# Kernel tuning notes

Measured on AMD Instinct MI355X. Metric: run time of the kernel, lower is better.

Reference implementation:

```python
import jax, jax.numpy as jnp
import numpy as np

N = 50000        # nodes
E = 800000       # edges (edge-nodes of the line graph)
LGE = 1600000    # line-graph edges
F_NODE = 256     # node feature dim
T = 64           # timestamp/edge feature dim
HID = 128        # hidden size
OUT = 64         # out size
SLOPE = 0.2      # leaky relu negative slope used in EdgeGCN / attention


def _glorot(key, shape):
    lim = jnp.sqrt(6.0 / (shape[0] + shape[1]))
    return jax.random.uniform(key, shape, jnp.float32, -lim, lim)


def setup_inputs() -> dict:
    key = jax.random.key(0)
    ks = jax.random.split(key, 24)
    inp = {
        "x": jax.random.normal(ks[0], (N, F_NODE), jnp.float32),
        "et": jax.random.normal(ks[1], (E, T), jnp.float32),
        "H": jax.random.randint(ks[2], (2, E), 0, N),
        "raw_edge_index": jax.random.randint(ks[3], (2, E), 0, N),
        "lg_edge_index": jax.random.randint(ks[4], (2, LGE), 0, E),
        # TSAEncoder: two SAGE-style layers on the line graph (T->HID->HID)
        "W_tsa1_s": _glorot(ks[5], (T, HID)),
        "W_tsa1_n": _glorot(ks[6], (T, HID)),
        "W_tsa2_s": _glorot(ks[7], (HID, HID)),
        "W_tsa2_n": _glorot(ks[8], (HID, HID)),
        # EdgeToNodeConv + EdgeGCN output linear
        "W_etn": _glorot(ks[9], (HID, HID)),
        "W_eg_lin": _glorot(ks[10], (HID, HID)),
        # edge_aggr SAGE (num_layers-1 = 1 layer)
        "W_ea_s": _glorot(ks[11], (HID, HID)),
        "W_ea_n": _glorot(ks[12], (HID, HID)),
        # attr_node_model SAGE (2 layers)
        "W_an1_s": _glorot(ks[13], (F_NODE, HID)),
        "W_an1_n": _glorot(ks[14], (F_NODE, HID)),
        "W_an2_s": _glorot(ks[15], (HID, HID)),
        "W_an2_n": _glorot(ks[16], (HID, HID)),
        # MixAttention
        "Wq": _glorot(ks[17], (HID, HID)),
        "Wk": _glorot(ks[18], (HID, HID)),
        "Wv": _glorot(ks[19], (HID, HID)),
        # final classifier
        "W_out": _glorot(ks[20], (HID, OUT)),
    }
    return inp


def _sage(h, src, dst, Ws, Wn, n):
    # mean-aggregator SAGE conv: self transform + mean of in-neighbors
    deg = jnp.clip(jax.ops.segment_sum(jnp.ones(src.shape[0], h.dtype), dst, num_segments=n), 1.0)
    nbr = jax.ops.segment_sum(h[src], dst, num_segments=n) / deg[:, None]
    return h @ Ws + nbr @ Wn


def reference(x, et, H, raw_edge_index, lg_edge_index,
              W_tsa1_s, W_tsa1_n, W_tsa2_s, W_tsa2_n,
              W_etn, W_eg_lin, W_ea_s, W_ea_n,
              W_an1_s, W_an1_n, W_an2_s, W_an2_n,
              Wq, Wk, Wv, W_out):
    src_lg, dst_lg = lg_edge_index[0], lg_edge_index[1]
    src, dst = raw_edge_index[0], raw_edge_index[1]

    # ---- EdgeGCN: TSAEncoder over line graph (edges as nodes) ----
    h = jax.nn.relu(_sage(et, src_lg, dst_lg, W_tsa1_s, W_tsa1_n, E))
    h = _sage(h, src_lg, dst_lg, W_tsa2_s, W_tsa2_n, E)          # [E, HID]

    # ---- EdgeToNodeConv: scatter edge reprs to both incident nodes (mean) ----
    ones_e = jnp.ones(E, h.dtype)
    agg = (jax.ops.segment_sum(h, H[0], num_segments=N)
           + jax.ops.segment_sum(h, H[1], num_segments=N))        # [N, HID]
    deg = jnp.clip(jax.ops.segment_sum(ones_e, H[0], num_segments=N)
                   + jax.ops.segment_sum(ones_e, H[1], num_segments=N), 1.0)
    node_e = (agg / deg[:, None]) @ W_etn
    edge_repr = jax.nn.leaky_relu(node_e, negative_slope=SLOPE) @ W_eg_lin  # [N, HID]

    # ---- edge_aggr: 1-layer SAGE over raw graph ----
    aggr_edge = _sage(edge_repr, src, dst, W_ea_s, W_ea_n, N)     # [N, HID]

    # ---- attr_node_model: 2-layer SAGE ----
    hn = jax.nn.relu(_sage(x, src, dst, W_an1_s, W_an1_n, N))
    hn = _sage(hn, src, dst, W_an2_s, W_an2_n, N)                 # [N, HID]

    # ---- MixAttention: edge-indexed cross attention (node queries, edge-repr keys/values) ----
    q = hn @ Wq
    k = aggr_edge @ Wk
    v = aggr_edge @ Wv
    score = jax.nn.leaky_relu(
        jnp.sum(q[dst] * k[src], axis=-1) / jnp.sqrt(jnp.asarray(HID, q.dtype)),
        negative_slope=SLOPE)                                     # [E]
    m = jax.ops.segment_max(score, dst, num_segments=N)
    m = jnp.where(jnp.isfinite(m), m, 0.0)
    ex = jnp.exp(score - m[dst])
    den = jnp.clip(jax.ops.segment_sum(ex, dst, num_segments=N), 1e-9)
    alpha = ex / den[dst]
    out = hn + jax.ops.segment_sum(alpha[:, None] * v[src], dst, num_segments=N)

    return jax.nn.log_softmax(out @ W_out, axis=1)                # [N, OUT]
```

## Files before the change

### kernel.cpp

```cpp
#include <hip/hip_runtime.h>
#include <cstddef>

static constexpr int Nn   = 50000;
static constexpr int Ee   = 800000;
static constexpr int LGEe = 1600000;

typedef __attribute__((ext_vector_type(8))) short bf16x8;
typedef __attribute__((ext_vector_type(4))) float f32x4;

__device__ __forceinline__ float bf2f(unsigned int u16) {
  return __uint_as_float(u16 << 16);
}
__device__ __forceinline__ unsigned int f2bf(float f) {
  unsigned int u = __float_as_uint(f);
  u += 0x7fffu + ((u >> 16) & 1u);
  return u >> 16;
}

__global__ __launch_bounds__(256)
void k_count_direct(const int* __restrict__ idx, int* __restrict__ cnt, int n) {
  int i = blockIdx.x * 256 + threadIdx.x;
  if (i < n) atomicAdd(&cnt[idx[i]], 1);
}
__global__ __launch_bounds__(256)
void k_count_comp(const int* __restrict__ Hrow, const int* __restrict__ dlg,
                  int* __restrict__ cnt, int n) {
  int i = blockIdx.x * 256 + threadIdx.x;
  if (i < n) atomicAdd(&cnt[Hrow[dlg[i]]], 1);
}
__global__ __launch_bounds__(256)
void k_scan1(const int* __restrict__ in, int* __restrict__ out,
             int* __restrict__ bsum, int n) {
  __shared__ int sd[256];
  int tid = threadIdx.x;
  int base = blockIdx.x * 1024 + tid * 4;
  int4 v = {0, 0, 0, 0};
  if (base < n) v = *(const int4*)(in + base);
  int s = v.x + v.y + v.z + v.w;
  sd[tid] = s; __syncthreads();
  for (int off = 1; off < 256; off <<= 1) {
    int t_ = (tid >= off) ? sd[tid - off] : 0; __syncthreads();
    sd[tid] += t_; __syncthreads();
  }
  int excl = sd[tid] - s;
  if (base < n) {
    int4 o; o.x = excl; o.y = o.x + v.x; o.z = o.y + v.y; o.w = o.z + v.z;
    *(int4*)(out + base) = o;
  }
  if (tid == 255) bsum[blockIdx.x] = sd[255];
}
__global__ __launch_bounds__(1024)
void k_scan2(int* __restrict__ b, int nb) {
  __shared__ int sd[1024];
  int tid = threadIdx.x;
  int v = (tid < nb) ? b[tid] : 0;
  sd[tid] = v; __syncthreads();
  for (int off = 1; off < 1024; off <<= 1) {
    int t_ = (tid >= off) ? sd[tid - off] : 0; __syncthreads();
    sd[tid] += t_; __syncthreads();
  }
  if (tid < nb) b[tid] = sd[tid] - v;
}
__global__ __launch_bounds__(256)
void k_scan3(int* __restrict__ out, const int* __restrict__ bsum, int n, int total) {
  int i = blockIdx.x * 256 + threadIdx.x;
  if (i < n) out[i] += bsum[i >> 10];
  if (i == 0) out[n] = total;
}
__global__ __launch_bounds__(256)
void k_fillA(const int* __restrict__ dlg, const int* __restrict__ slg,
             const int* __restrict__ ptr, int* __restrict__ cur,
             int* __restrict__ ent, int n) {
  int m = blockIdx.x * 256 + threadIdx.x;
  if (m >= n) return;
  int d = dlg[m];
  int pos = ptr[d] + atomicAdd(&cur[d], 1);
  ent[pos] = slg[m];
}
__global__ __launch_bounds__(256)
void k_fillB(const int* __restrict__ Hrow, const int* __restrict__ dlg,
             const int* __restrict__ slg, const int* __restrict__ ptrA,
             const int* __restrict__ ptrB, int* __restrict__ cur,
             int* __restrict__ entS, float* __restrict__ entW, int n) {
  int m = blockIdx.x * 256 + threadIdx.x;
  if (m >= n) return;
  int d = dlg[m];
  int seg = Hrow[d];
  int pos = ptrB[seg] + atomicAdd(&cur[seg], 1);
  entS[pos] = slg[m];
  int la = ptrA[d + 1] - ptrA[d];
  entW[pos] = 1.0f / (float)max(la, 1);
}
__global__ __launch_bounds__(256)
void k_fillC(const int* __restrict__ Hrow, const int* __restrict__ ptr,
             int* __restrict__ cur, int* __restrict__ ent, int n) {
  int e = blockIdx.x * 256 + threadIdx.x;
  if (e >= n) return;
  int seg = Hrow[e];
  int pos = ptr[seg] + atomicAdd(&cur[seg], 1);
  ent[pos] = e;
}
__global__ __launch_bounds__(256)
void k_fillD(const int* __restrict__ dstA, const int* __restrict__ srcA,
             const int* __restrict__ ptr, int* __restrict__ cur,
             int* __restrict__ ent, int n) {
  int e = blockIdx.x * 256 + threadIdx.x;
  if (e >= n) return;
  int seg = dstA[e];
  int pos = ptr[seg] + atomicAdd(&cur[seg], 1);
  ent[pos] = srcA[e];
}
__global__ __launch_bounds__(256)
void k_rdeg(const int* __restrict__ ptr, float* __restrict__ r, int n) {
  int i = blockIdx.x * 256 + threadIdx.x;
  if (i < n) r[i] = 1.0f / fmaxf((float)(ptr[i + 1] - ptr[i]), 1.0f);
}

__global__ __launch_bounds__(256)
void k_gemm128(int M, const float* __restrict__ A, int K,
               const float* __restrict__ W, const float* __restrict__ dgA,
               int reluA, int act, float* __restrict__ C, int beta)
{
  __shared__ float sA[32][132];
  __shared__ float sW[32][132];
  const int t = threadIdx.x, tr = t >> 4, tc = t & 15;
  const int row0 = blockIdx.x * 128;
  float acc[8][8];
  #pragma unroll
  for (int i = 0; i < 8; ++i)
    #pragma unroll
    for (int j = 0; j < 8; ++j) acc[i][j] = 0.f;

  #pragma unroll 1
  for (int k0 = 0; k0 < K; k0 += 32) {
    __syncthreads();
    #pragma unroll
    for (int j = 0; j < 4; ++j) {
      int idx = t * 4 + j * 1024;
      int r = idx >> 5, kk = idx & 31;
      int gr = row0 + r; if (gr > M - 1) gr = M - 1;
      float4 va = *(const float4*)(A + (size_t)gr * K + k0 + kk);
      if (reluA) {
        va.x = fmaxf(va.x, 0.f); va.y = fmaxf(va.y, 0.f);
        va.z = fmaxf(va.z, 0.f); va.w = fmaxf(va.w, 0.f);
      }
      if (dgA) {
        float sc = dgA[gr];
        va.x *= sc; va.y *= sc; va.z *= sc; va.w *= sc;
      }
      sA[kk + 0][r] = va.x; sA[kk + 1][r] = va.y;
      sA[kk + 2][r] = va.z; sA[kk + 3][r] = va.w;
    }
    #pragma unroll
    for (int j = 0; j < 4; ++j) {
      int idx = t * 4 + j * 1024;
      int kk = idx >> 7, c = idx & 127;
      *(float4*)&sW[kk][c] = *(const float4*)(W + (size_t)(k0 + kk) * 128 + c);
    }
    __syncthreads();
    #pragma unroll
    for (int kk = 0; kk < 32; ++kk) {
      float a[8], w[8];
      *(float4*)&a[0] = *(const float4*)&sA[kk][tr * 4];
      *(float4*)&a[4] = *(const float4*)&sA[kk][64 + tr * 4];
      *(float4*)&w[0] = *(const float4*)&sW[kk][tc * 4];
      *(float4*)&w[4] = *(const float4*)&sW[kk][64 + tc * 4];
      #pragma unroll
      for (int i = 0; i < 8; ++i)
        #pragma unroll
        for (int j = 0; j < 8; ++j)
          acc[i][j] = fmaf(a[i], w[j], acc[i][j]);
    }
  }
  #pragma unroll 1
  for (int i = 0; i < 8; ++i) {
    int gr = row0 + (i & 4) * 16 + tr * 4 + (i & 3);
    if (gr >= M) continue;
    float o[8];
    #pragma unroll
    for (int j = 0; j < 8; ++j) {
      float vv = acc[i][j];
      if (act == 1)      vv = fmaxf(vv, 0.f);
      else if (act == 2) vv = vv > 0.f ? vv : vv * 0.2f;
      o[j] = vv;
    }
    float* p = C + (size_t)gr * 128;
    if (beta) {
      float4 c0 = *(const float4*)(p + tc * 4), c1 = *(const float4*)(p + 64 + tc * 4);
      o[0] += c0.x; o[1] += c0.y; o[2] += c0.z; o[3] += c0.w;
      o[4] += c1.x; o[5] += c1.y; o[6] += c1.z; o[7] += c1.w;
    }
    *(float4*)(p + tc * 4)      = *(const float4*)&o[0];
    *(float4*)(p + 64 + tc * 4) = *(const float4*)&o[4];
  }
}

__global__ __launch_bounds__(256)
void k_tsa1(const float* __restrict__ et,
            const int* __restrict__ rp, const int* __restrict__ ent,
            const float* __restrict__ Ws, const float* __restrict__ Wn,
            unsigned short* __restrict__ BUF)
{
  __shared__ __align__(16) unsigned char smem[34816];
  unsigned short* sAh = (unsigned short*)smem;
  unsigned short* sAl = (unsigned short*)(smem + 16384);
  int*   sEnt  = (int*)(smem + 32768);
  float* stage = (float*)smem;

  const int t = threadIdx.x, wv = t >> 6, lane = t & 63;
  const int tr = t >> 4, tc = t & 15;
  const int nrow = lane & 15, kg = lane >> 4;
  const int seg0 = blockIdx.x * 64;
  const int segbase = seg0 + wv * 16;

  int rpv = (lane <= 16) ? rp[segbase + lane] : 0;
  int nxtv = __shfl(rpv, (lane + 1) & 63);
  float invv = 1.f / fmaxf((float)(nxtv - rpv), 1.f);

  const int base = rp[seg0];
  const int cnt  = rp[seg0 + 64] - base;
  const int lim  = cnt < 512 ? cnt : 512;
  for (int i = t; i < lim; i += 256) sEnt[i] = ent[base + i];

  {
    float dv[16];
    #pragma unroll
    for (int i = 0; i < 16; ++i)
      dv[i] = et[(size_t)(segbase + i) * 64 + lane];
    #pragma unroll
    for (int i = 0; i < 16; ++i) {
      int ss = wv * 16 + i;
      unsigned int hi = f2bf(dv[i]);
      float lo = dv[i] - bf2f(hi);
      int idx = ss * 128 + (lane ^ ((ss & 7) << 3));
      sAh[idx] = (unsigned short)hi;
      sAl[idx] = (unsigned short)f2bf(lo);
    }
  }

  bf16x8 Bh[2][4], Bl[2][4];
  #pragma unroll
  for (int np = 0; np < 2; ++np) {
    int n = (wv * 2 + np) * 16 + nrow;
    #pragma unroll
    for (int kc = 0; kc < 4; ++kc) {
      const float* Wp = (kc < 2) ? Ws : Wn;
      int kr0 = (kc & 1) * 32 + kg * 8;
      #pragma unroll
      for (int j = 0; j < 8; ++j) {
        float w = Wp[(size_t)(kr0 + j) * 128 + n];
        unsigned int hi = f2bf(w);
        float lo = w - bf2f(hi);
        Bh[np][kc][j] = (short)(unsigned short)hi;
        Bl[np][kc][j] = (short)(unsigned short)f2bf(lo);
      }
    }
  }
  __syncthreads();

  {
    int q0 = __shfl(rpv, 0);
    int q1 = __shfl(rpv, 16);
    int c = 0;
    int b_next = __shfl(rpv, 1);
    float idg = __shfl(invv, 0);
    float a = 0.f;
    #pragma unroll 1
    for (int j = q0; j < q1; j += 8) {
      float x[8];
      #pragma unroll
      for (int u = 0; u < 8; ++u) {
        int jj = j + u; jj = jj < q1 ? jj : q1 - 1;
        int ix = jj - base;
        int s = (ix < 512) ? sEnt[ix] : ent[jj];
        x[u] = et[(size_t)s * 64 + lane];
      }
      #pragma unroll
      for (int u = 0; u < 8; ++u) {
        int jj = j + u;
        if (jj >= q1) break;
        while (jj >= b_next) {
          float v = a * idg;
          int ss = wv * 16 + c;
          unsigned int hi = f2bf(v);
          float lo = v - bf2f(hi);
          int idx = ss * 128 + ((64 + lane) ^ ((ss & 7) << 3));
          sAh[idx] = (unsigned short)hi;
          sAl[idx] = (unsigned short)f2bf(lo);
          a = 0.f;
          ++c;
          b_next = __shfl(rpv, c + 1);
          idg = __shfl(invv, c);
        }
        a += x[u];
      }
    }
    #pragma unroll 1
    for (;;) {
      float v = a * idg;
      int ss = wv * 16 + c;
      unsigned int hi = f2bf(v);
      float lo = v - bf2f(hi);
      int idx = ss * 128 + ((64 + lane) ^ ((ss & 7) << 3));
      sAh[idx] = (unsigned short)hi;
      sAl[idx] = (unsigned short)f2bf(lo);
      a = 0.f;
      if (++c >= 16) break;
      idg = __shfl(invv, c);
    }
  }
  __syncthreads();

  f32x4 acc[4][2];
  #pragma unroll
  for (int m = 0; m < 4; ++m)
    #pragma unroll
    for (int np = 0; np < 2; ++np)
      acc[m][np] = (f32x4){0.f, 0.f, 0.f, 0.f};

  #pragma unroll
  for (int kc = 0; kc < 4; ++kc) {
    #pragma unroll
    for (int m = 0; m < 4; ++m) {
      int ss = m * 16 + nrow;
      int kbase = kc * 32 + kg * 8;
      int idx = ss * 128 + (kbase ^ ((ss & 7) << 3));
      bf16x8 ah = *(const bf16x8*)(sAh + idx);
      bf16x8 al = *(const bf16x8*)(sAl + idx);
      #pragma unroll
      for (int np = 0; np < 2; ++np) {
        acc[m][np] = __builtin_amdgcn_mfma_f32_16x16x32_bf16(ah, Bh[np][kc], acc[m][np], 0, 0, 0);
        acc[m][np] = __builtin_amdgcn_mfma_f32_16x16x32_bf16(al, Bh[np][kc], acc[m][np], 0, 0, 0);
        acc[m][np] = __builtin_amdgcn_mfma_f32_16x16x32_bf16(ah, Bl[np][kc], acc[m][np], 0, 0, 0);
      }
    }
  }

  __syncthreads();
  #pragma unroll
  for (int m = 0; m < 4; ++m)
    #pragma unroll
    for (int np = 0; np < 2; ++np)
      #pragma unroll
      for (int r = 0; r < 4; ++r)
        stage[(m * 16 + kg * 4 + r) * 132 + (wv * 2 + np) * 16 + nrow] = acc[m][np][r];
  __syncthreads();
  #pragma unroll
  for (int i = 0; i < 4; ++i) {
    int s = tr * 4 + i;
    const float* sp = stage + s * 132 + tc * 8;
    float4 v0 = *(const float4*)sp;
    float4 v1 = *(const float4*)(sp + 4);
    unsigned int pk[4];
    pk[0] = f2bf(v0.x) | (f2bf(v0.y) << 16);
    pk[1] = f2bf(v0.z) | (f2bf(v0.w) << 16);
    pk[2] = f2bf(v1.x) | (f2bf(v1.y) << 16);
    pk[3] = f2bf(v1.z) | (f2bf(v1.w) << 16);
    uint4 st = {pk[0], pk[1], pk[2], pk[3]};
    *(uint4*)(BUF + (size_t)(seg0 + s) * 128 + tc * 8) = st;
  }
}

__global__ __launch_bounds__(256)
void k_poolb(const int* __restrict__ rp, const int* __restrict__ ent,
             const float* __restrict__ entw,
             const unsigned short* __restrict__ SRC,
             float* __restrict__ O, int nseg, int total)
{
  const int wv = threadIdx.x >> 6, lane = threadIdx.x & 63;
  const int chunk = blockIdx.x * 4 + wv;
  const int c0 = chunk * 256;
  if (c0 >= total) return;
  int c1 = c0 + 256; if (c1 > total) c1 = total;

  int lo = 0, hi = nseg;
  while (lo + 1 < hi) {
    int mid = (lo + hi) >> 1;
    if (rp[mid] <= c0) lo = mid; else hi = mid;
  }
  int seg = lo;
  int sstart = rp[seg];
  int send = rp[seg + 1];
  float a0 = 0.f, a1 = 0.f;

  #pragma unroll 1
  for (int j = c0; j < c1; j += 8) {
    int ids[8]; float w[8];
    #pragma unroll
    for (int u = 0; u < 8; ++u) {
      int jj = j + u; jj = jj < c1 ? jj : c1 - 1;
      ids[u] = ent[jj];
      w[u] = entw ? entw[jj] : 1.f;
    }
    unsigned int uv[8];
    #pragma unroll
    for (int u = 0; u < 8; ++u)
      uv[u] = *(const unsigned int*)(SRC + (size_t)ids[u] * 128 + 2 * lane);
    #pragma unroll
    for (int u = 0; u < 8; ++u) {
      int jj = j + u;
      if (jj >= c1) break;
      while (jj >= send) {
        float* p = O + (size_t)seg * 128;
        if (sstart >= c0 && send <= c1) {
          p[2 * lane]     += a0;
          p[2 * lane + 1] += a1;
        } else {
          atomicAdd(p + 2 * lane, a0);
          atomicAdd(p + 2 * lane + 1, a1);
        }
        a0 = a1 = 0.f;
        ++seg; sstart = send; send = rp[seg + 1];
      }
      a0 = fmaf(w[u], fmaxf(bf2f(uv[u] & 0xffffu), 0.f), a0);
      a1 = fmaf(w[u], fmaxf(bf2f(uv[u] >> 16),     0.f), a1);
    }
  }
  {
    float* p = O + (size_t)seg * 128;
    if (sstart >= c0 && send <= c1) {
      p[2 * lane]     += a0;
      p[2 * lane + 1] += a1;
    } else {
      atomicAdd(p + 2 * lane, a0);
      atomicAdd(p + 2 * lane + 1, a1);
    }
  }
}

__global__ __launch_bounds__(256)
void k_poolf(const int* __restrict__ rp, const int* __restrict__ ent,
             const float* __restrict__ SRC, float* __restrict__ O,
             int nseg, int total)
{
  const int wv = threadIdx.x >> 6, lane = threadIdx.x & 63;
  const int chunk = blockIdx.x * 4 + wv;
  const int c0 = chunk * 256;
  if (c0 >= total) return;
  int c1 = c0 + 256; if (c1 > total) c1 = total;

  int lo = 0, hi = nseg;
  while (lo + 1 < hi) {
    int mid = (lo + hi) >> 1;
    if (rp[mid] <= c0) lo = mid; else hi = mid;
  }
  int seg = lo;
  int sstart = rp[seg];
  int send = rp[seg + 1];
  float a0 = 0.f, a1 = 0.f;

  #pragma unroll 1
  for (int j = c0; j < c1; j += 8) {
    int ids[8];
    #pragma unroll
    for (int u = 0; u < 8; ++u) {
      int jj = j + u; jj = jj < c1 ? jj : c1 - 1;
      ids[u] = ent[jj];
    }
    float2 v[8];
    #pragma unroll
    for (int u = 0; u < 8; ++u)
      v[u] = ((const float2*)(SRC + (size_t)ids[u] * 128))[lane];
    #pragma unroll
    for (int u = 0; u < 8; ++u) {
      int jj = j + u;
      if (jj >= c1) break;
      while (jj >= send) {
        float sc = 1.f / fmaxf((float)(send - sstart), 1.f);
        float* p = O + (size_t)seg * 128;
        if (sstart >= c0 && send <= c1) {
          p[2 * lane]     += a0 * sc;
          p[2 * lane + 1] += a1 * sc;
        } else {
          atomicAdd(p + 2 * lane, a0 * sc);
          atomicAdd(p + 2 * lane + 1, a1 * sc);
        }
        a0 = a1 = 0.f;
        ++seg; sstart = send; send = rp[seg + 1];
      }
      a0 += v[u].x; a1 += v[u].y;
    }
  }
  {
    float sc = 1.f / fmaxf((float)(send - sstart), 1.f);
    float* p = O + (size_t)seg * 128;
    if (sstart >= c0 && send <= c1) {
      p[2 * lane]     += a0 * sc;
      p[2 * lane + 1] += a1 * sc;
    } else {
      atomicAdd(p + 2 * lane, a0 * sc);
      atomicAdd(p + 2 * lane + 1, a1 * sc);
    }
  }
}

__global__ __launch_bounds__(256)
void k_attn(const int* __restrict__ rp, const int* __restrict__ ent,
            const float* __restrict__ q, const float* __restrict__ kb,
            const float* __restrict__ vb, float* __restrict__ o, int nseg)
{
  int wv = threadIdx.x >> 6, lane = threadIdx.x & 63;
  int seg = blockIdx.x * 4 + wv;
  if (seg >= nseg) return;
  int p0 = rp[seg], p1 = rp[seg + 1];
  if (p0 >= p1) return;
  float2 q2 = ((const float2*)(q + (size_t)seg * 128))[lane];
  float m = -1e30f, l = 0.f, o0 = 0.f, o1 = 0.f;
  #pragma unroll 1
  for (int j = p0; j < p1; j += 4) {
    int s[4];
    #pragma unroll
    for (int i = 0; i < 4; ++i) {
      int jj = j + i; jj = jj < p1 ? jj : p1 - 1;
      s[i] = ent[jj];
    }
    float2 k2[4], v2[4];
    #pragma unroll
    for (int i = 0; i < 4; ++i)
      k2[i] = ((const float2*)(kb + (size_t)s[i] * 128))[lane];
    #pragma unroll
    for (int i = 0; i < 4; ++i)
      v2[i] = ((const float2*)(vb + (size_t)s[i] * 128))[lane];
    float d[4];
    #pragma unroll
    for (int i = 0; i < 4; ++i) d[i] = fmaf(q2.x, k2[i].x, q2.y * k2[i].y);
    #pragma unroll
    for (int off = 1; off < 64; off <<= 1) {
      #pragma unroll
      for (int i = 0; i < 4; ++i) d[i] += __shfl_xor(d[i], off);
    }
    float sc[4];
    #pragma unroll
    for (int i = 0; i < 4; ++i) {
      float v = d[i] * 0.088388347648318447f;
      v = v > 0.f ? v : 0.2f * v;
      sc[i] = (j + i < p1) ? v : -1e30f;
    }
    float mb = fmaxf(fmaxf(sc[0], sc[1]), fmaxf(sc[2], sc[3]));
    float mn = fmaxf(m, mb);
    float scale = expf(m - mn);
    float e[4];
    #pragma unroll
    for (int i = 0; i < 4; ++i)
      e[i] = (j + i < p1) ? expf(sc[i] - mn) : 0.f;
    l  = l  * scale + ((e[0] + e[1]) + (e[2] + e[3]));
    o0 = o0 * scale + ((e[0] * v2[0].x + e[1] * v2[1].x) + (e[2] * v2[2].x + e[3] * v2[3].x));
    o1 = o1 * scale + ((e[0] * v2[0].y + e[1] * v2[1].y) + (e[2] * v2[2].y + e[3] * v2[3].y));
    m = mn;
  }
  float inv = 1.f / fmaxf(l, 1e-9f);
  float2* orow = (float2*)(o + (size_t)seg * 128);
  float2 cur = orow[lane];
  cur.x += o0 * inv; cur.y += o1 * inv;
  orow[lane] = cur;
}

__global__ __launch_bounds__(256)
void k_out(const float* __restrict__ attn, const float* __restrict__ Wout,
           float* __restrict__ out, int n) {
  __shared__ float sW[128 * 64];
  for (int i = threadIdx.x; i < 128 * 64; i += 256) sW[i] = Wout[i];
  __syncthreads();
  int wave = threadIdx.x >> 6, lane = threadIdx.x & 63;
  int row = blockIdx.x * 4 + wave;
  if (row >= n) return;
  const float* a = attn + (size_t)row * 128;
  float z = 0.f;
  #pragma unroll 8
  for (int k = 0; k < 128; ++k) z = fmaf(a[k], sW[k * 64 + lane], z);
  float mx = z;
  #pragma unroll
  for (int off = 32; off; off >>= 1) mx = fmaxf(mx, __shfl_xor(mx, off));
  float ee = expf(z - mx);
  float ss = ee;
  #pragma unroll
  for (int off = 32; off; off >>= 1) ss += __shfl_xor(ss, off);
  out[(size_t)row * 64 + lane] = z - mx - logf(ss);
}

extern "C" void kernel_launch(void* const* d_in, const int* in_sizes, int n_in,
                              void* d_out, int out_size, void* d_ws, size_t ws_size,
                              hipStream_t stream) {
  (void)in_sizes; (void)n_in; (void)out_size;
  const float* x        = (const float*)d_in[0];
  const float* et       = (const float*)d_in[1];
  const int*   H0       = (const int*)d_in[2];
  const int*   H1       = H0 + Ee;
  const int*   src      = (const int*)d_in[3];
  const int*   dst      = src + Ee;
  const int*   src_lg   = (const int*)d_in[4];
  const int*   dst_lg   = src_lg + LGEe;
  const float* W_tsa1_s = (const float*)d_in[5];
  const float* W_tsa1_n = (const float*)d_in[6];
  const float* W_tsa2_s = (const float*)d_in[7];
  const float* W_tsa2_n = (const float*)d_in[8];
  const float* W_etn    = (const float*)d_in[9];
  const float* W_eg_lin = (const float*)d_in[10];
  const float* W_ea_s   = (const float*)d_in[11];
  const float* W_ea_n   = (const float*)d_in[12];
  const float* W_an1_s  = (const float*)d_in[13];
  const float* W_an1_n  = (const float*)d_in[14];
  const float* W_an2_s  = (const float*)d_in[15];
  const float* W_an2_n  = (const float*)d_in[16];
  const float* Wq       = (const float*)d_in[17];
  const float* Wk       = (const float*)d_in[18];
  const float* Wv       = (const float*)d_in[19];
  const float* W_out    = (const float*)d_in[20];
  float* out = (float*)d_out;

  char* wp = (char*)d_ws;
  size_t avail = ws_size;
  auto alloc = [&](size_t bytes) -> void* {
    void* r = (void*)wp;
    size_t pad = (bytes + 255) & ~(size_t)255;
    wp += pad; avail = (avail >= pad) ? avail - pad : 0;
    return r;
  };
  const size_t NH = (size_t)Nn * 128;
  unsigned short* BUF = (unsigned short*)alloc((size_t)Ee * 128 * 2);
  float* agg   = (float*)alloc(NH * 4);
  int* ptrA  = (int*)alloc(((size_t)Ee + 1) * 4);
  int* cntA  = (int*)alloc((size_t)Ee * 4);
  int* entA  = (int*)alloc((size_t)LGEe * 4);
  int* ptrB  = (int*)alloc(((size_t)Nn + 1) * 4);
  int* cntB  = (int*)alloc((size_t)Nn * 4);
  int* entBs = (int*)alloc((size_t)2 * LGEe * 4);
  float* entBw = (float*)alloc((size_t)2 * LGEe * 4);
  int* ptrC  = (int*)alloc(((size_t)Nn + 1) * 4);
  int* cntC  = (int*)alloc((size_t)Nn * 4);
  int* entC  = (int*)alloc((size_t)2 * Ee * 4);
  int* ptrD  = (int*)alloc(((size_t)Nn + 1) * 4);
  int* cntD  = (int*)alloc((size_t)Nn * 4);
  int* entD  = (int*)alloc((size_t)Ee * 4);
  float* rdegN = (float*)alloc((size_t)Nn * 4);
  int* bsum  = (int*)alloc(2048 * 4);
  if (avail == 0 && wp > (char*)d_ws + ws_size) return;

  float* er  = (float*)BUF + 0 * NH;
  float* ae  = (float*)BUF + 1 * NH;
  float* hn  = (float*)BUF + 2 * NH;
  float* hn2 = (float*)BUF + 3 * NH;
  float* qb  = (float*)BUF + 4 * NH;
  float* kb  = (float*)BUF + 5 * NH;
  float* vb  = (float*)BUF + 6 * NH;
  float* tmp = (float*)BUF + 7 * NH;
  float* T = (float*)entBs;

  auto cdiv = [](long a, long b) { return (int)((a + b - 1) / b); };
  auto scan = [&](int* cnt, int* ptr, int n, int total) {
    int nb = cdiv(n, 1024);
    k_scan1<<<nb, 256, 0, stream>>>(cnt, ptr, bsum, n);
    k_scan2<<<1, 1024, 0, stream>>>(bsum, nb);
    k_scan3<<<cdiv(n, 256), 256, 0, stream>>>(ptr, bsum, n, total);
  };

  const int gLG = cdiv(LGEe, 256), gEe = cdiv(Ee, 256);

  hipMemsetAsync(cntA, 0, (size_t)Ee * 4, stream);
  k_count_direct<<<gLG, 256, 0, stream>>>(dst_lg, cntA, LGEe);
  scan(cntA, ptrA, Ee, LGEe);
  hipMemsetAsync(cntA, 0, (size_t)Ee * 4, stream);
  k_fillA<<<gLG, 256, 0, stream>>>(dst_lg, src_lg, ptrA, cntA, entA, LGEe);

  hipMemsetAsync(cntB, 0, (size_t)Nn * 4, stream);
  k_count_comp<<<gLG, 256, 0, stream>>>(H0, dst_lg, cntB, LGEe);
  k_count_comp<<<gLG, 256, 0, stream>>>(H1, dst_lg, cntB, LGEe);
  scan(cntB, ptrB, Nn, 2 * LGEe);
  hipMemsetAsync(cntB, 0, (size_t)Nn * 4, stream);
  k_fillB<<<gLG, 256, 0, stream>>>(H0, dst_lg, src_lg, ptrA, ptrB, cntB, entBs, entBw, LGEe);
  k_fillB<<<gLG, 256, 0, stream>>>(H1, dst_lg, src_lg, ptrA, ptrB, cntB, entBs, entBw, LGEe);

  hipMemsetAsync(cntC, 0, (size_t)Nn * 4, stream);
  k_count_direct<<<gEe, 256, 0, stream>>>(H0, cntC, Ee);
  k_count_direct<<<gEe, 256, 0, stream>>>(H1, cntC, Ee);
  scan(cntC, ptrC, Nn, 2 * Ee);
  hipMemsetAsync(cntC, 0, (size_t)Nn * 4, stream);
  k_fillC<<<gEe, 256, 0, stream>>>(H0, ptrC, cntC, entC, Ee);
  k_fillC<<<gEe, 256, 0, stream>>>(H1, ptrC, cntC, entC, Ee);

  hipMemsetAsync(cntD, 0, (size_t)Nn * 4, stream);
  k_count_direct<<<gEe, 256, 0, stream>>>(dst, cntD, Ee);
  scan(cntD, ptrD, Nn, Ee);
  hipMemsetAsync(cntD, 0, (size_t)Nn * 4, stream);
  k_fillD<<<gEe, 256, 0, stream>>>(dst, src, ptrD, cntD, entD, Ee);
  k_rdeg<<<cdiv(Nn, 256), 256, 0, stream>>>(ptrC, rdegN, Nn);

  const int gN128 = cdiv(Nn, 128);
  const int gW    = cdiv(Nn, 4);
  const int gP2   = cdiv(cdiv(2 * LGEe, 256), 4);
  const int gP1   = cdiv(cdiv(2 * Ee, 256), 4);
  const int gPf   = cdiv(cdiv(Ee, 256), 4);

  k_tsa1<<<Ee / 64, 256, 0, stream>>>(et, ptrA, entA, W_tsa1_s, W_tsa1_n, BUF);

  hipMemsetAsync(agg, 0, NH * 4, stream);
  k_poolb<<<gP2, 256, 0, stream>>>(ptrB, entBs, entBw, BUF, agg, Nn, 2 * LGEe);
  k_gemm128<<<gN128, 256, 0, stream>>>(Nn, agg, 128, W_tsa2_n, nullptr, 0, 0, T, 0);
  hipMemsetAsync(agg, 0, NH * 4, stream);
  k_poolb<<<gP1, 256, 0, stream>>>(ptrC, entC, nullptr, BUF, agg, Nn, 2 * Ee);
  k_gemm128<<<gN128, 256, 0, stream>>>(Nn, agg, 128, W_tsa2_s, nullptr, 0, 0, T, 1);
  k_gemm128<<<gN128, 256, 0, stream>>>(Nn, T, 128, W_etn, rdegN, 0, 2, tmp, 0);
  k_gemm128<<<gN128, 256, 0, stream>>>(Nn, tmp, 128, W_eg_lin, nullptr, 0, 0, er, 0);

  k_gemm128<<<gN128, 256, 0, stream>>>(Nn, er, 128, W_ea_s, nullptr, 0, 0, ae, 0);
  k_gemm128<<<gN128, 256, 0, stream>>>(Nn, er, 128, W_ea_n, nullptr, 0, 0, tmp, 0);
  k_poolf<<<gPf, 256, 0, stream>>>(ptrD, entD, tmp, ae, Nn, Ee);

  k_gemm128<<<gN128, 256, 0, stream>>>(Nn, x, 256, W_an1_s, nullptr, 0, 0, hn, 0);
  k_gemm128<<<gN128, 256, 0, stream>>>(Nn, x, 256, W_an1_n, nullptr, 0, 0, tmp, 0);
  k_poolf<<<gPf, 256, 0, stream>>>(ptrD, entD, tmp, hn, Nn, Ee);
  k_gemm128<<<gN128, 256, 0, stream>>>(Nn, hn, 128, W_an2_s, nullptr, 1, 0, hn2, 0);
  k_gemm128<<<gN128, 256, 0, stream>>>(Nn, hn, 128, W_an2_n, nullptr, 1, 0, tmp, 0);
  k_poolf<<<gPf, 256, 0, stream>>>(ptrD, entD, tmp, hn2, Nn, Ee);

  k_gemm128<<<gN128, 256, 0, stream>>>(Nn, hn2, 128, Wq, nullptr, 0, 0, qb, 0);
  k_gemm128<<<gN128, 256, 0, stream>>>(Nn, ae, 128, Wk, nullptr, 0, 0, kb, 0);
  k_gemm128<<<gN128, 256, 0, stream>>>(Nn, ae, 128, Wv, nullptr, 0, 0, vb, 0);
  k_attn<<<gW, 256, 0, stream>>>(ptrD, entD, qb, kb, vb, hn2, Nn);

  k_out<<<gW, 256, 0, stream>>>(hn2, W_out, out, Nn);
}
```

Measured before the change: 2.812 ms.

## Replace FP32 SIMT GEMMs with split-bf16 MFMA kernel and fuse paired GEMMs

Swaps the scalar FP32 128x128-tiled GEMM for a kernel that runs 16x16x32 bf16 MFMA instructions. Each FP32 operand is split into a bf16 high part and a bf16 residual, and three MFMAs per step recover near-FP32 accuracy. A DUAL template variant multiplies the same A tile by two weight matrices, so the paired self/neighbor and K/V GEMMs read A once and need fewer launches. Weights are reloaded from global memory and split again in every block, which adds conversion overhead, and the result carries a small precision risk compared with plain FP32.

```diff
diff --git a/kernel.cpp b/kernel.cpp
--- a/kernel.cpp
+++ b/kernel.cpp
@@ -116,30 +116,79 @@
   if (i < n) r[i] = 1.0f / fmaxf((float)(ptr[i + 1] - ptr[i]), 1.0f);
 }
 
-__global__ __launch_bounds__(256)
-void k_gemm128(int M, const float* __restrict__ A, int K,
-               const float* __restrict__ W, const float* __restrict__ dgA,
-               int reluA, int act, float* __restrict__ C, int beta)
+#define MG_SWEEP(WP, ACC)                                                       \
+  {                                                                             \
+    bf16x8 Bh[2][4], Bl[2][4];                                                  \
+    _Pragma("unroll")                                                           \
+    for (int np = 0; np < 2; ++np) {                                            \
+      int n = (wv * 2 + np) * 16 + nrow;                                        \
+      _Pragma("unroll")                                                         \
+      for (int kc = 0; kc < 4; ++kc) {                                          \
+        int kr0 = kh * 128 + kc * 32 + kg * 8;                                  \
+        _Pragma("unroll")                                                       \
+        for (int j = 0; j < 8; ++j) {                                           \
+          float w = (WP)[(size_t)(kr0 + j) * 128 + n];                          \
+          unsigned int hi = f2bf(w);                                            \
+          float lo = w - bf2f(hi);                                              \
+          Bh[np][kc][j] = (short)(unsigned short)hi;                            \
+          Bl[np][kc][j] = (short)(unsigned short)f2bf(lo);                      \
+        }                                                                       \
+      }                                                                         \
+    }                                                                           \
+    _Pragma("unroll")                                                           \
+    for (int kc = 0; kc < 4; ++kc) {                                            \
+      _Pragma("unroll")                                                         \
+      for (int m = 0; m < 4; ++m) {                                             \
+        int ss = m * 16 + nrow;                                                 \
+        int idx = ss * 128 + ((kc * 32 + kg * 8) ^ ((ss & 7) << 3));            \
+        bf16x8 ah = *(const bf16x8*)(sAh + idx);                                \
+        bf16x8 al = *(const bf16x8*)(sAl + idx);                                \
+        _Pragma("unroll")                                                       \
+        for (int np = 0; np < 2; ++np) {                                        \
+          ACC[m][np] = __builtin_amdgcn_mfma_f32_16x16x32_bf16(ah, Bh[np][kc], ACC[m][np], 0, 0, 0); \
+          ACC[m][np] = __builtin_amdgcn_mfma_f32_16x16x32_bf16(al, Bh[np][kc], ACC[m][np], 0, 0, 0); \
+          ACC[m][np] = __builtin_amdgcn_mfma_f32_16x16x32_bf16(ah, Bl[np][kc], ACC[m][np], 0, 0, 0); \
+        }                                                                       \
+      }                                                                         \
+    }                                                                           \
+  }
+
+template <int DUAL>
+__global__ __launch_bounds__(256)
+void k_mgemm(int M, const float* __restrict__ A, int K,
+             const float* __restrict__ W1, const float* __restrict__ W2,
+             const float* __restrict__ dgA, int reluA, int act,
+             float* __restrict__ C1, float* __restrict__ C2, int beta1)
 {
-  __shared__ float sA[32][132];
-  __shared__ float sW[32][132];
-  const int t = threadIdx.x, tr = t >> 4, tc = t & 15;
-  const int row0 = blockIdx.x * 128;
-  float acc[8][8];
-  #pragma unroll
-  for (int i = 0; i < 8; ++i)
-    #pragma unroll
-    for (int j = 0; j < 8; ++j) acc[i][j] = 0.f;
-
+  __shared__ __align__(16) unsigned char smem[34816];
+  unsigned short* sAh = (unsigned short*)smem;
+  unsigned short* sAl = (unsigned short*)(smem + 16384);
+  float* stage = (float*)smem;
+
+  const int t = threadIdx.x, wv = t >> 6, lane = t & 63;
+  const int tr = t >> 4, tc = t & 15;
+  const int nrow = lane & 15, kg = lane >> 4;
+  const int row0 = blockIdx.x * 64;
+
+  f32x4 acc1[4][2], acc2[4][2];
+  #pragma unroll
+  for (int m = 0; m < 4; ++m)
+    #pragma unroll
+    for (int np = 0; np < 2; ++np) {
+      acc1[m][np] = (f32x4){0.f, 0.f, 0.f, 0.f};
+      if (DUAL) acc2[m][np] = (f32x4){0.f, 0.f, 0.f, 0.f};
+    }
+
+  const int nkh = K >> 7;
   #pragma unroll 1
-  for (int k0 = 0; k0 < K; k0 += 32) {
-    __syncthreads();
-    #pragma unroll
-    for (int j = 0; j < 4; ++j) {
-      int idx = t * 4 + j * 1024;
-      int r = idx >> 5, kk = idx & 31;
+  for (int kh = 0; kh < nkh; ++kh) {
+    if (kh) __syncthreads();
+    #pragma unroll
+    for (int j = 0; j < 8; ++j) {
+      int idx = t + j * 256;
+      int r = idx >> 5, c4 = idx & 31;
       int gr = row0 + r; if (gr > M - 1) gr = M - 1;
-      float4 va = *(const float4*)(A + (size_t)gr * K + k0 + kk);
+      float4 va = *(const float4*)(A + (size_t)gr * K + kh * 128 + c4 * 4);
       if (reluA) {
         va.x = fmaxf(va.x, 0.f); va.y = fmaxf(va.y, 0.f);
         va.z = fmaxf(va.z, 0.f); va.w = fmaxf(va.w, 0.f);
@@ -148,50 +197,85 @@
         float sc = dgA[gr];
         va.x *= sc; va.y *= sc; va.z *= sc; va.w *= sc;
       }
-      sA[kk + 0][r] = va.x; sA[kk + 1][r] = va.y;
-      sA[kk + 2][r] = va.z; sA[kk + 3][r] = va.w;
-    }
-    #pragma unroll
-    for (int j = 0; j < 4; ++j) {
-      int idx = t * 4 + j * 1024;
-      int kk = idx >> 7, c = idx & 127;
-      *(float4*)&sW[kk][c] = *(const float4*)(W + (size_t)(k0 + kk) * 128 + c);
+      float v[4] = {va.x, va.y, va.z, va.w};
+      unsigned int h[4], l[4];
+      #pragma unroll
+      for (int q = 0; q < 4; ++q) {
+        h[q] = f2bf(v[q]);
+        l[q] = f2bf(v[q] - bf2f(h[q]));
+      }
+      int bidx = r * 128 + ((c4 * 4) ^ ((r & 7) << 3));
+      uint2 ph = {h[0] | (h[1] << 16), h[2] | (h[3] << 16)};
+      uint2 pl = {l[0] | (l[1] << 16), l[2] | (l[3] << 16)};
+      *(uint2*)(sAh + bidx) = ph;
+      *(uint2*)(sAl + bidx) = pl;
     }
     __syncthreads();
-    #pragma unroll
-    for (int kk = 0; kk < 32; ++kk) {
-      float a[8], w[8];
-      *(float4*)&a[0] = *(const float4*)&sA[kk][tr * 4];
-      *(float4*)&a[4] = *(const float4*)&sA[kk][64 + tr * 4];
-      *(float4*)&w[0] = *(const float4*)&sW[kk][tc * 4];
-      *(float4*)&w[4] = *(const float4*)&sW[kk][64 + tc * 4];
-      #pragma unroll
-      for (int i = 0; i < 8; ++i)
-        #pragma unroll
-        for (int j = 0; j < 8; ++j)
-          acc[i][j] = fmaf(a[i], w[j], acc[i][j]);
-    }
-  }
-  #pragma unroll 1
-  for (int i = 0; i < 8; ++i) {
-    int gr = row0 + (i & 4) * 16 + tr * 4 + (i & 3);
+
+    MG_SWEEP(W1, acc1);
+    if (DUAL) MG_SWEEP(W2, acc2);
+  }
+
+  __syncthreads();
+  #pragma unroll
+  for (int m = 0; m < 4; ++m)
+    #pragma unroll
+    for (int np = 0; np < 2; ++np)
+      #pragma unroll
+      for (int r = 0; r < 4; ++r)
+        stage[(m * 16 + kg * 4 + r) * 132 + (wv * 2 + np) * 16 + nrow] = acc1[m][np][r];
+  __syncthreads();
+  #pragma unroll
+  for (int i = 0; i < 4; ++i) {
+    int s = tr * 4 + i, gr = row0 + s;
     if (gr >= M) continue;
-    float o[8];
-    #pragma unroll
-    for (int j = 0; j < 8; ++j) {
-      float vv = acc[i][j];
+    const float* sp = stage + s * 132 + tc * 8;
+    float4 v0 = *(const float4*)sp, v1 = *(const float4*)(sp + 4);
+    float o[8] = {v0.x, v0.y, v0.z, v0.w, v1.x, v1.y, v1.z, v1.w};
+    #pragma unroll
+    for (int j2 = 0; j2 < 8; ++j2) {
+      float vv = o[j2];
       if (act == 1)      vv = fmaxf(vv, 0.f);
-      else if (act == 2) vv = vv > 0.f ? vv : vv * 0.2f;
-      o[j] = vv;
-    }
-    float* p = C + (size_t)gr * 128;
-    if (beta) {
-      float4 c0 = *(const float4*)(p + tc * 4), c1 = *(const float4*)(p + 64 + tc * 4);
+      else if (act == 2) vv = vv > 0.f ? vv : 0.2f * vv;
+      o[j2] = vv;
+    }
+    float* p = C1 + (size_t)gr * 128 + tc * 8;
+    if (beta1) {
+      float4 c0 = *(const float4*)p, c1 = *(const float4*)(p + 4);
       o[0] += c0.x; o[1] += c0.y; o[2] += c0.z; o[3] += c0.w;
       o[4] += c1.x; o[5] += c1.y; o[6] += c1.z; o[7] += c1.w;
     }
-    *(float4*)(p + tc * 4)      = *(const float4*)&o[0];
-    *(float4*)(p + 64 + tc * 4) = *(const float4*)&o[4];
+    *(float4*)p       = *(const float4*)&o[0];
+    *(float4*)(p + 4) = *(const float4*)&o[4];
+  }
+  if (DUAL) {
+    __syncthreads();
+    #pragma unroll
+    for (int m = 0; m < 4; ++m)
+      #pragma unroll
+      for (int np = 0; np < 2; ++np)
+        #pragma unroll
+        for (int r = 0; r < 4; ++r)
+          stage[(m * 16 + kg * 4 + r) * 132 + (wv * 2 + np) * 16 + nrow] = acc2[m][np][r];
+    __syncthreads();
+    #pragma unroll
+    for (int i = 0; i < 4; ++i) {
+      int s = tr * 4 + i, gr = row0 + s;
+      if (gr >= M) continue;
+      const float* sp = stage + s * 132 + tc * 8;
+      float4 v0 = *(const float4*)sp, v1 = *(const float4*)(sp + 4);
+      float o[8] = {v0.x, v0.y, v0.z, v0.w, v1.x, v1.y, v1.z, v1.w};
+      #pragma unroll
+      for (int j2 = 0; j2 < 8; ++j2) {
+        float vv = o[j2];
+        if (act == 1)      vv = fmaxf(vv, 0.f);
+        else if (act == 2) vv = vv > 0.f ? vv : 0.2f * vv;
+        o[j2] = vv;
+      }
+      float* p = C2 + (size_t)gr * 128 + tc * 8;
+      *(float4*)p       = *(const float4*)&o[0];
+      *(float4*)(p + 4) = *(const float4*)&o[4];
+    }
   }
 }
 
@@ -685,7 +769,7 @@
   k_fillD<<<gEe, 256, 0, stream>>>(dst, src, ptrD, cntD, entD, Ee);
   k_rdeg<<<cdiv(Nn, 256), 256, 0, stream>>>(ptrC, rdegN, Nn);
 
-  const int gN128 = cdiv(Nn, 128);
+  const int gM64  = cdiv(Nn, 64);
   const int gW    = cdiv(Nn, 4);
   const int gP2   = cdiv(cdiv(2 * LGEe, 256), 4);
   const int gP1   = cdiv(cdiv(2 * Ee, 256), 4);
@@ -695,27 +779,23 @@
 
   hipMemsetAsync(agg, 0, NH * 4, stream);
   k_poolb<<<gP2, 256, 0, stream>>>(ptrB, entBs, entBw, BUF, agg, Nn, 2 * LGEe);
-  k_gemm128<<<gN128, 256, 0, stream>>>(Nn, agg, 128, W_tsa2_n, nullptr, 0, 0, T, 0);
+  k_mgemm<0><<<gM64, 256, 0, stream>>>(Nn, agg, 128, W_tsa2_n, nullptr, nullptr, 0, 0, T, nullptr, 0);
   hipMemsetAsync(agg, 0, NH * 4, stream);
   k_poolb<<<gP1, 256, 0, stream>>>(ptrC, entC, nullptr, BUF, agg, Nn, 2 * Ee);
-  k_gemm128<<<gN128, 256, 0, stream>>>(Nn, agg, 128, W_tsa2_s, nullptr, 0, 0, T, 1);
-  k_gemm128<<<gN128, 256, 0, stream>>>(Nn, T, 128, W_etn, rdegN, 0, 2, tmp, 0);
-  k_gemm128<<<gN128, 256, 0, stream>>>(Nn, tmp, 128, W_eg_lin, nullptr, 0, 0, er, 0);
-
-  k_gemm128<<<gN128, 256, 0, stream>>>(Nn, er, 128, W_ea_s, nullptr, 0, 0, ae, 0);
-  k_gemm128<<<gN128, 256, 0, stream>>>(Nn, er, 128, W_ea_n, nullptr, 0, 0, tmp, 0);
+  k_mgemm<0><<<gM64, 256, 0, stream>>>(Nn, agg, 128, W_tsa2_s, nullptr, nullptr, 0, 0, T, nullptr, 1);
+  k_mgemm<0><<<gM64, 256, 0, stream>>>(Nn, T, 128, W_etn, nullptr, rdegN, 0, 2, tmp, nullptr, 0);
+  k_mgemm<0><<<gM64, 256, 0, stream>>>(Nn, tmp, 128, W_eg_lin, nullptr, nullptr, 0, 0, er, nullptr, 0);
+
+  k_mgemm<1><<<gM64, 256, 0, stream>>>(Nn, er, 128, W_ea_s, W_ea_n, nullptr, 0, 0, ae, tmp, 0);
   k_poolf<<<gPf, 256, 0, stream>>>(ptrD, entD, tmp, ae, Nn, Ee);
 
-  k_gemm128<<<gN128, 256, 0, stream>>>(Nn, x, 256, W_an1_s, nullptr, 0, 0, hn, 0);
-  k_gemm128<<<gN128, 256, 0, stream>>>(Nn, x, 256, W_an1_n, nullptr, 0, 0, tmp, 0);
+  k_mgemm<1><<<gM64, 256, 0, stream>>>(Nn, x, 256, W_an1_s, W_an1_n, nullptr, 0, 0, hn, tmp, 0);
   k_poolf<<<gPf, 256, 0, stream>>>(ptrD, entD, tmp, hn, Nn, Ee);
-  k_gemm128<<<gN128, 256, 0, stream>>>(Nn, hn, 128, W_an2_s, nullptr, 1, 0, hn2, 0);
-  k_gemm128<<<gN128, 256, 0, stream>>>(Nn, hn, 128, W_an2_n, nullptr, 1, 0, tmp, 0);
+  k_mgemm<1><<<gM64, 256, 0, stream>>>(Nn, hn, 128, W_an2_s, W_an2_n, nullptr, 1, 0, hn2, tmp, 0);
   k_poolf<<<gPf, 256, 0, stream>>>(ptrD, entD, tmp, hn2, Nn, Ee);
 
-  k_gemm128<<<gN128, 256, 0, stream>>>(Nn, hn2, 128, Wq, nullptr, 0, 0, qb, 0);
-  k_gemm128<<<gN128, 256, 0, stream>>>(Nn, ae, 128, Wk, nullptr, 0, 0, kb, 0);
-  k_gemm128<<<gN128, 256, 0, stream>>>(Nn, ae, 128, Wv, nullptr, 0, 0, vb, 0);
+  k_mgemm<0><<<gM64, 256, 0, stream>>>(Nn, hn2, 128, Wq, nullptr, nullptr, 0, 0, qb, nullptr, 0);
+  k_mgemm<1><<<gM64, 256, 0, stream>>>(Nn, ae, 128, Wk, Wv, nullptr, 0, 0, kb, vb, 0);
   k_attn<<<gW, 256, 0, stream>>>(ptrD, entD, qb, kb, vb, hn2, Nn);
 
   k_out<<<gW, 256, 0, stream>>>(hn2, W_out, out, Nn);
```

Result: faster. 2.302 ms (-18.1%).
